# Optimization experiments

Measured on AMD Instinct MI355X. Metric: run time of the kernel, lower is better.

Reference implementation:

```python
import jax, jax.numpy as jnp
import numpy as np

BINS = 256
EPS = 1e-8


def _norm255(x):
    # (x - min) / (max - min) * 255, truncated to int (torch .int())
    mx = jnp.max(x, axis=(2, 3), keepdims=True)
    mn = jnp.min(x, axis=(2, 3), keepdims=True)
    return ((x - mn) / (mx - mn) * 255.0).astype(jnp.int32)


def _hist256(x):
    # x int32 [B,C,H,W] -> per-(b,c) 256-bin histogram [B,C,256] float32
    B, C = x.shape[0], x.shape[1]
    flat = x.reshape(B * C, -1)
    rows = jnp.arange(B * C)[:, None]
    h = jnp.zeros((B * C, BINS), jnp.float32).at[rows, flat].add(1.0)
    return h.reshape(B, C, BINS)


def _entropy(x):
    # faithful to Entropy(): p = hist / (H*W); h = -sum p*log(p+1e-8)
    B, C, H, W = x.shape
    p = _hist256(x) / (H * W)
    h = -jnp.sum(p * jnp.log(p + EPS), axis=2)
    return h[:, :, None, None]  # [B,C,1,1]


def _joint_entropy(x_p, x_ms):
    # Faithful to Joint_entropy's quirky count: for each (i,j) it counts pixels
    # where (x_ms==i AND x_p==j) OR (x_ms!=i AND x_p!=j).
    # count[i,j] = 2*J[i,j] + npix - hist_ms[i] - hist_p[j], J = joint histogram.
    B, C, H, W = x_ms.shape
    npix = H * W
    bins = jnp.arange(BINS)
    M = (x_ms.reshape(B, C, npix)[..., None] == bins).astype(jnp.float32)  # [B,C,P,256]
    P = (x_p.reshape(B, npix)[..., None] == bins).astype(jnp.float32)      # [B,P,256]
    J = jnp.einsum('bcpi,bpj->bcij', M, P)                                  # [B,C,256,256]
    hist_ms = jnp.sum(M, axis=2)  # [B,C,256]
    hist_p = jnp.sum(P, axis=1)   # [B,256]
    count = 2.0 * J + npix - hist_ms[:, :, :, None] - hist_p[:, None, None, :]
    p = count / float(BINS * BINS)  # original divides by 256*256, not npix
    h = -jnp.sum(p * jnp.log(p + EPS), axis=(2, 3))
    return h[:, :, None, None]  # [B,C,1,1]


def _channel(f_p, f_ms):
    B, C, H, W = f_p.shape
    f_p_m = jnp.mean(f_p, axis=1, keepdims=True)  # [B,1,H,W]
    # AdaptiveAvgPool2d((16,16)) with H,W divisible by 16 == block mean
    pooled = f_p.reshape(B, C, 16, H // 16, 16, W // 16).mean(axis=(3, 5))
    f_p_a = jnp.mean(pooled, axis=1, keepdims=True)  # [B,1,16,16]
    f_ms_n = _norm255(f_ms)
    f_p_m_n = _norm255(f_p_m)
    f_p_a_n = _norm255(f_p_a)
    h_ms = _entropy(f_ms_n)                 # [B,C,1,1]
    h_p = _entropy(f_p_m_n)                 # [B,1,1,1]
    h_ms_p = _joint_entropy(f_p_a_n, f_ms_n)  # [B,C,1,1]
    mi = h_p + h_ms - h_ms_p
    mi = jax.nn.softmax(mi, axis=1)  # nn.Softmax() on 4D -> dim=1
    return f_ms + f_ms * mi


def _similarity(f_p, f_ms):
    B, C, H, W = f_p.shape
    f_ms_u = jax.image.resize(f_ms, (B, C, H, W), method='bilinear')
    a = f_ms_u.reshape(B, C, -1)
    b = f_p.reshape(B, C, -1)
    a = a - jnp.mean(a, axis=2, keepdims=True)
    b = b - jnp.mean(b, axis=2, keepdims=True)
    na = jnp.sqrt(jnp.sum(a * a, axis=2))  # [B,C] (ms norms)
    nb = jnp.sqrt(jnp.sum(b * b, axis=2))  # [B,C] (p norms)
    s = jnp.einsum('bcp,bdp->bcd', a, b)   # [B,C,C]
    return s / ((na * nb) / 100.0)[:, :, None]


def _spatial(f_p, f_ms):
    B, C, H, W = f_p.shape
    s_m = _similarity(f_p, f_ms)
    mx = jnp.max(s_m, axis=2)        # [B,C]
    idx = jnp.argmax(s_m, axis=2)    # [B,C] best f_p channel per ms channel
    scores = jax.nn.softmax(mx, axis=1)
    brow = jnp.arange(B)[:, None]
    # group score: sum of softmax scores of ms-channels that picked value v
    g = jnp.zeros((B, C), scores.dtype).at[brow, idx].add(scores)
    cnt = jnp.zeros((B, C), jnp.int32).at[brow, idx].add(1)
    k = jnp.min(jnp.sum(cnt > 0, axis=1))  # min #unique over batch
    min_k = (k + 1) // 2                   # ceil(min_k / 2)
    order = jnp.argsort(-g, axis=1)        # descending group score; absent groups (0) sort last
    sorted_scores = jnp.take_along_axis(g, order, axis=1)  # [B,C]
    pos_mask = jnp.arange(C) < min_k       # keep top min_k positions
    z = jnp.where(pos_mask[None, :], sorted_scores, -jnp.inf)
    w = jax.nn.softmax(z, axis=1)          # softmax over selected scores, 0 elsewhere
    gathered = jnp.take_along_axis(f_p, order[:, :, None, None], axis=1)  # [B,C,H,W]
    mask = jnp.sum(w[:, :, None, None] * jax.nn.sigmoid(gathered), axis=1, keepdims=True)
    return f_p + f_p * mask


def setup_inputs() -> dict:
    key = jax.random.key(0)
    k1, k2 = jax.random.split(key)
    f_p = jax.random.normal(k1, (8, 64, 256, 256), dtype=jnp.float32)
    f_ms = jax.random.normal(k2, (8, 64, 16, 16), dtype=jnp.float32)
    return {"f_p": f_p, "f_ms": f_ms}


def reference(f_p, f_ms):
    rel_ms = _channel(f_p, f_ms)
    rel_p = _spatial(f_p, f_ms)
    return (rel_p, rel_ms)
```

## Files before the change

### kernel.cpp

```cpp
#include <hip/hip_runtime.h>

#define BB 8
#define CC 64
#define HP 256
#define WP 256
#define PP 65536
#define QQ 256

__device__ __forceinline__ unsigned encF(float f) {
    unsigned u = __float_as_uint(f);
    return (u & 0x80000000u) ? ~u : (u | 0x80000000u);
}
__device__ __forceinline__ float decF(unsigned u) {
    unsigned b = (u & 0x80000000u) ? (u ^ 0x80000000u) : ~u;
    return __uint_as_float(b);
}

__device__ __forceinline__ double blockSumD(double v, double* red4) {
    int t = threadIdx.x;
    for (int d = 32; d; d >>= 1) v += __shfl_down(v, d, 64);
    __syncthreads();
    if ((t & 63) == 0) red4[t >> 6] = v;
    __syncthreads();
    double r = red4[0] + red4[1] + red4[2] + red4[3];
    __syncthreads();
    return r;
}

__global__ void k0_init(unsigned* minmax, int* histpm) {
    int t = threadIdx.x + blockIdx.x * blockDim.x;
    if (t < BB) { minmax[2 * t] = 0xFFFFFFFFu; minmax[2 * t + 1] = 0u; }
    if (t < BB * 256) histpm[t] = 0;
}

__global__ __launch_bounds__(256) void k1_fpm(const float* __restrict__ fp,
                                              float* __restrict__ fpm,
                                              unsigned* __restrict__ minmax) {
    int b = blockIdx.y;
    int i4 = blockIdx.x * 256 + threadIdx.x;
    const float4* src = (const float4*)(fp + (size_t)b * CC * PP);
    float sx = 0.f, sy = 0.f, sz = 0.f, sw = 0.f;
#pragma unroll 8
    for (int c = 0; c < CC; ++c) {
        float4 v = src[(size_t)c * (PP / 4) + i4];
        sx += v.x; sy += v.y; sz += v.z; sw += v.w;
    }
    const float inv = 1.0f / 64.0f;
    float4 m; m.x = sx * inv; m.y = sy * inv; m.z = sz * inv; m.w = sw * inv;
    ((float4*)(fpm + (size_t)b * PP))[i4] = m;
    float mn = fminf(fminf(m.x, m.y), fminf(m.z, m.w));
    float mx = fmaxf(fmaxf(m.x, m.y), fmaxf(m.z, m.w));
    for (int d = 32; d; d >>= 1) {
        mn = fminf(mn, __shfl_down(mn, d, 64));
        mx = fmaxf(mx, __shfl_down(mx, d, 64));
    }
    __shared__ unsigned smn, smx;
    if (threadIdx.x == 0) { smn = 0xFFFFFFFFu; smx = 0u; }
    __syncthreads();
    if ((threadIdx.x & 63) == 0) { atomicMin(&smn, encF(mn)); atomicMax(&smx, encF(mx)); }
    __syncthreads();
    if (threadIdx.x == 0) { atomicMin(&minmax[2 * b], smn); atomicMax(&minmax[2 * b + 1], smx); }
}

__global__ __launch_bounds__(256) void k2a_hist(const float* __restrict__ fpm,
                                                const unsigned* __restrict__ minmax,
                                                int* __restrict__ histpm) {
    int b = blockIdx.y;
    __shared__ int h[256];
    h[threadIdx.x] = 0;
    __syncthreads();
    float mn = decF(minmax[2 * b]);
    float mx = decF(minmax[2 * b + 1]);
    float dd = mx - mn;
    int i4 = blockIdx.x * 256 + threadIdx.x;
    float4 v = ((const float4*)(fpm + (size_t)b * PP))[i4];
    int b0 = (int)((v.x - mn) / dd * 255.0f);
    int b1 = (int)((v.y - mn) / dd * 255.0f);
    int b2 = (int)((v.z - mn) / dd * 255.0f);
    int b3 = (int)((v.w - mn) / dd * 255.0f);
    b0 = min(max(b0, 0), 255); b1 = min(max(b1, 0), 255);
    b2 = min(max(b2, 0), 255); b3 = min(max(b3, 0), 255);
    atomicAdd(&h[b0], 1); atomicAdd(&h[b1], 1);
    atomicAdd(&h[b2], 1); atomicAdd(&h[b3], 1);
    __syncthreads();
    atomicAdd(&histpm[b * 256 + threadIdx.x], h[threadIdx.x]);
}

__global__ __launch_bounds__(256) void k2b_entropy(const int* __restrict__ histpm,
                                                   float* __restrict__ hpE) {
    __shared__ double red4[4];
    int b = blockIdx.x;
    int n = histpm[b * 256 + threadIdx.x];
    float p = (float)n * (1.0f / 65536.0f);
    double term = -(double)(p * __logf(p + 1e-8f));
    double h = blockSumD(term, red4);
    if (threadIdx.x == 0) hpE[b] = (float)h;
}

__global__ __launch_bounds__(256) void k3_chan(const float* __restrict__ fp,
                                               float* __restrict__ cellsum,
                                               float* __restrict__ gtent,
                                               float* __restrict__ chsum,
                                               float* __restrict__ chsumsq) {
    int blk = blockIdx.x, b = blk >> 6, c = blk & 63;
    int x = threadIdx.x, s = x >> 4, r = x & 15;
    const float* src = fp + (size_t)(b * CC + c) * PP;
    __shared__ float tentL[256];
    __shared__ double red4[4];
    tentL[x] = 0.0f;
    __syncthreads();
    float wm, w0, wp;
    if (x <= 7)        { wm = 0.f; w0 = 1.f; wp = 0.f; }
    else if (x >= 248) { wm = 0.f; w0 = 1.f; wp = 0.f; }
    else if (r < 8)    { float fx = ((float)r + 8.5f) * 0.0625f; wm = 1.f - fx; w0 = fx;       wp = 0.f; }
    else               { float fx = ((float)r - 7.5f) * 0.0625f; wm = 0.f;      w0 = 1.f - fx; wp = fx;  }
    double sum = 0.0, ssq = 0.0;
    for (int q = 0; q < 16; ++q) {
        float am = 0.f, a0 = 0.f, ap = 0.f, cs = 0.f;
#pragma unroll
        for (int ry = 0; ry < 16; ++ry) {
            float v = src[(q * 16 + ry) * 256 + x];
            sum += (double)v;
            ssq += (double)v * (double)v;
            cs  += v;
            if ((q == 0 && ry < 8) || (q == 15 && ry >= 8)) {
                a0 += v;
            } else if (ry < 8) {
                float fy = ((float)ry + 8.5f) * 0.0625f;
                am += (1.f - fy) * v; a0 += fy * v;
            } else {
                float fy = ((float)ry - 7.5f) * 0.0625f;
                a0 += (1.f - fy) * v; ap += fy * v;
            }
        }
        float vals[10];
        vals[0] = am * wm; vals[1] = am * w0; vals[2] = am * wp;
        vals[3] = a0 * wm; vals[4] = a0 * w0; vals[5] = a0 * wp;
        vals[6] = ap * wm; vals[7] = ap * w0; vals[8] = ap * wp;
        vals[9] = cs;
#pragma unroll
        for (int d = 8; d; d >>= 1) {
#pragma unroll
            for (int k2 = 0; k2 < 10; ++k2) vals[k2] += __shfl_down(vals[k2], d, 16);
        }
        if (r == 0) {
            if (q > 0) {
                if (s > 0)  atomicAdd(&tentL[(q - 1) * 16 + (s - 1)], vals[0]);
                atomicAdd(&tentL[(q - 1) * 16 + s], vals[1]);
                if (s < 15) atomicAdd(&tentL[(q - 1) * 16 + (s + 1)], vals[2]);
            }
            if (s > 0)  atomicAdd(&tentL[q * 16 + (s - 1)], vals[3]);
            atomicAdd(&tentL[q * 16 + s], vals[4]);
            if (s < 15) atomicAdd(&tentL[q * 16 + (s + 1)], vals[5]);
            if (q < 15) {
                if (s > 0)  atomicAdd(&tentL[(q + 1) * 16 + (s - 1)], vals[6]);
                atomicAdd(&tentL[(q + 1) * 16 + s], vals[7]);
                if (s < 15) atomicAdd(&tentL[(q + 1) * 16 + (s + 1)], vals[8]);
            }
            cellsum[(size_t)(b * CC + c) * QQ + q * 16 + s] = vals[9];
        }
    }
    __syncthreads();
    gtent[(size_t)(b * CC + c) * QQ + x] = tentL[x];
    double st = blockSumD(sum, red4);
    double sq = blockSumD(ssq, red4);
    if (x == 0) { chsum[b * CC + c] = (float)st; chsumsq[b * CC + c] = (float)sq; }
}

__global__ __launch_bounds__(256) void k4_ms(const float* __restrict__ fms,
                                             int* __restrict__ msn,
                                             int* __restrict__ histms,
                                             float* __restrict__ hmsE,
                                             float* __restrict__ naArr,
                                             float* __restrict__ mssum) {
    int blk = blockIdx.x, b = blk >> 6, c = blk & 63, t = threadIdx.x;
    __shared__ float m[256];
    __shared__ int hist[256];
    __shared__ double red4[4];
    __shared__ double U[256];
    __shared__ unsigned umn, umx;
    float v = fms[(size_t)(b * CC + c) * QQ + t];
    m[t] = v;
    hist[t] = 0;
    if (t == 0) { umn = 0xFFFFFFFFu; umx = 0u; }
    float mn = v, mx = v;
    for (int d = 32; d; d >>= 1) {
        mn = fminf(mn, __shfl_down(mn, d, 64));
        mx = fmaxf(mx, __shfl_down(mx, d, 64));
    }
    __syncthreads();
    if ((t & 63) == 0) { atomicMin(&umn, encF(mn)); atomicMax(&umx, encF(mx)); }
    __syncthreads();
    mn = decF(umn); mx = decF(umx);
    int bin = (int)((v - mn) / (mx - mn) * 255.0f);
    bin = min(max(bin, 0), 255);
    msn[(size_t)(b * CC + c) * QQ + t] = bin;
    atomicAdd(&hist[bin], 1);
    __syncthreads();
    histms[(size_t)(b * CC + c) * QQ + t] = hist[t];
    float pf = (float)hist[t] * (1.0f / 256.0f);
    double term = -(double)(pf * __logf(pf + 1e-8f));
    double h = blockSumD(term, red4);
    if (t == 0) hmsE[b * CC + c] = (float)h;
    int i = t >> 4, j = t & 15;
    double kdj = (j == 0 || j == 15) ? 13.328125 : 10.65625;
    double mv = (double)m[t];
    double uu = kdj * mv + 2.671875 * ((j > 0 ? (double)m[t - 1] : 0.0) +
                                       (j < 15 ? (double)m[t + 1] : 0.0));
    U[t] = uu;
    __syncthreads();
    double kdi = (i == 0 || i == 15) ? 13.328125 : 10.65625;
    double vv = kdi * U[t] + 2.671875 * ((i > 0 ? U[t - 16] : 0.0) +
                                         (i < 15 ? U[t + 16] : 0.0));
    double sq = blockSumD(mv * vv, red4);
    double msm = blockSumD(mv, red4);
    if (t == 0) {
        mssum[b * CC + c] = (float)msm;
        double meanu = msm * (1.0 / 256.0);
        double na2 = sq - 65536.0 * meanu * meanu;
        naArr[b * CC + c] = (float)sqrt(na2 > 0.0 ? na2 : 0.0);
    }
}

__global__ __launch_bounds__(256) void k5_pa(const float* __restrict__ cellsum,
                                             int* __restrict__ pan,
                                             int* __restrict__ histp) {
    int b = blockIdx.x, t = threadIdx.x;
    __shared__ int hist[256];
    __shared__ unsigned umn, umx;
    hist[t] = 0;
    if (t == 0) { umn = 0xFFFFFFFFu; umx = 0u; }
    double acc = 0.0;
    for (int c = 0; c < CC; ++c) acc += (double)cellsum[(size_t)(b * CC + c) * QQ + t];
    float pa = (float)(acc * (1.0 / 256.0) * (1.0 / 64.0));
    float mn = pa, mx = pa;
    for (int d = 32; d; d >>= 1) {
        mn = fminf(mn, __shfl_down(mn, d, 64));
        mx = fmaxf(mx, __shfl_down(mx, d, 64));
    }
    __syncthreads();
    if ((t & 63) == 0) { atomicMin(&umn, encF(mn)); atomicMax(&umx, encF(mx)); }
    __syncthreads();
    mn = decF(umn); mx = decF(umx);
    int bin = (int)((pa - mn) / (mx - mn) * 255.0f);
    bin = min(max(bin, 0), 255);
    pan[b * QQ + t] = bin;
    atomicAdd(&hist[bin], 1);
    __syncthreads();
    histp[b * 256 + t] = hist[t];
}

__global__ __launch_bounds__(256) void k6_joint(const int* __restrict__ msn,
                                                const int* __restrict__ pan,
                                                const int* __restrict__ histms,
                                                const int* __restrict__ histp,
                                                float* __restrict__ hjoint) {
    int blk = blockIdx.x, b = blk >> 6, c = blk & 63, t = threadIdx.x;
    __shared__ int key[256], hms[256], hp[256];
    __shared__ double red4[4];
    int iv = msn[(size_t)(b * CC + c) * QQ + t];
    int jv = pan[b * QQ + t];
    key[t] = (iv << 8) | jv;
    hms[t] = histms[(size_t)(b * CC + c) * QQ + t];
    hp[t] = histp[b * 256 + t];
    __syncthreads();
    unsigned long long w0_ = 0, w1_ = 0, w2_ = 0, w3_ = 0;
    for (int p = 0; p < 256; ++p) {
        int k2 = key[p];
        if ((k2 >> 8) == t) {
            int j = k2 & 255;
            unsigned long long bit = 1ull << (j & 63);
            int w = j >> 6;
            if (w == 0) w0_ |= bit; else if (w == 1) w1_ |= bit;
            else if (w == 2) w2_ |= bit; else w3_ |= bit;
        }
    }
    double acc = 0.0;
    int basei = 256 - hms[t];
    unsigned long long words[4] = { w0_, w1_, w2_, w3_ };
#pragma unroll
    for (int w = 0; w < 4; ++w) {
        unsigned long long word = words[w];
        for (int jj = 0; jj < 64; ++jj) {
            if (!((word >> jj) & 1ull)) {
                int cnt = basei - hp[w * 64 + jj];
                float pf = (float)cnt * (1.0f / 65536.0f);
                acc -= (double)(pf * __logf(pf + 1e-8f));
            }
        }
    }
    int myk = key[t], n = 0; bool first = true;
    for (int p = 0; p < 256; ++p) {
        int k2 = key[p];
        if (k2 == myk) { n++; if (p < t) first = false; }
    }
    if (first) {
        int cnt = 2 * n + 256 - hms[myk >> 8] - hp[myk & 255];
        float pf = (float)cnt * (1.0f / 65536.0f);
        acc -= (double)(pf * __logf(pf + 1e-8f));
    }
    double h = blockSumD(acc, red4);
    if (t == 0) hjoint[b * CC + c] = (float)h;
}

__global__ __launch_bounds__(256) void k7_relms(const float* __restrict__ fms,
                                                const float* __restrict__ hmsE,
                                                const float* __restrict__ hpE,
                                                const float* __restrict__ hjoint,
                                                float* __restrict__ out2) {
    int b = blockIdx.x, t = threadIdx.x;
    __shared__ double mi[64];
    if (t < 64) mi[t] = (double)hpE[b] + (double)hmsE[b * CC + t] - (double)hjoint[b * CC + t];
    __syncthreads();
    if (t == 0) {
        double mxv = mi[0];
        for (int c2 = 1; c2 < 64; ++c2) if (mi[c2] > mxv) mxv = mi[c2];
        double s = 0.0;
        for (int c2 = 0; c2 < 64; ++c2) { mi[c2] = exp(mi[c2] - mxv); s += mi[c2]; }
        for (int c2 = 0; c2 < 64; ++c2) mi[c2] /= s;
    }
    __syncthreads();
    const float* src = fms + (size_t)b * CC * QQ;
    float* dst = out2 + (size_t)b * CC * QQ;
    for (int e = t; e < CC * QQ; e += 256) {
        float v = src[e];
        float miv = (float)mi[e >> 8];
        dst[e] = v + v * miv;
    }
}

__global__ __launch_bounds__(256) void k8_smax(const float* __restrict__ fms,
                                               const float* __restrict__ gtent,
                                               const float* __restrict__ mssum,
                                               const float* __restrict__ chsum,
                                               const float* __restrict__ chsumsq,
                                               const float* __restrict__ naArr,
                                               float* __restrict__ mxArr,
                                               int* __restrict__ idxArr) {
    int blk = blockIdx.x, b = blk >> 6, c = blk & 63, t = threadIdx.x;
    __shared__ float msrow[256];
    __shared__ double part[256];
    __shared__ double sval[64];
    msrow[t] = fms[(size_t)(b * CC + c) * QQ + t];
    __syncthreads();
    int d = t >> 2, pr = t & 3;
    const float* g = gtent + (size_t)(b * CC + d) * QQ + pr * 64;
    const float* mr = msrow + pr * 64;
    double acc = 0.0;
    for (int q2 = 0; q2 < 64; ++q2) acc += (double)mr[q2] * (double)g[q2];
    part[t] = acc;
    __syncthreads();
    if (t < 64) {
        double meanu = (double)mssum[b * CC + c] * (1.0 / 256.0);
        double meanp = (double)chsum[b * CC + t] * (1.0 / 65536.0);
        sval[t] = part[t * 4] + part[t * 4 + 1] + part[t * 4 + 2] + part[t * 4 + 3]
                  - 65536.0 * meanu * meanp;
    }
    __syncthreads();
    if (t == 0) {
        double best = sval[0]; int bi2 = 0;
        for (int dd = 1; dd < 64; ++dd) { if (sval[dd] > best) { best = sval[dd]; bi2 = dd; } }
        double nac = (double)naArr[b * CC + c];
        double sc_ = (double)chsum[b * CC + c];
        double sq_ = (double)chsumsq[b * CC + c];
        double nb2 = sq_ - sc_ * sc_ * (1.0 / 65536.0);
        double nbc = sqrt(nb2 > 0.0 ? nb2 : 0.0);
        mxArr[b * CC + c] = (float)(best * 100.0 / (nac * nbc));
        idxArr[b * CC + c] = bi2;
    }
}

__global__ __launch_bounds__(512) void k9_small(const float* __restrict__ mxArr,
                                                const int* __restrict__ idxArr,
                                                float* __restrict__ wsel,
                                                int* __restrict__ chanA,
                                                int* __restrict__ minkA) {
    __shared__ double sc[8][64];
    __shared__ double gs[8][64];
    __shared__ int idxS[8][64];
    __shared__ int ordv[8][64];
    __shared__ int uarr[8];
    __shared__ int mkS;
    int t = threadIdx.x;
    int b = t >> 6, c = t & 63;
    double v = (double)mxArr[b * 64 + c];
    double mx = v;
    for (int d = 32; d; d >>= 1) mx = fmax(mx, __shfl_down(mx, d, 64));
    mx = __shfl(mx, 0, 64);
    double e = exp(v - mx);
    double s = e;
    for (int d = 32; d; d >>= 1) s += __shfl_down(s, d, 64);
    s = __shfl(s, 0, 64);
    sc[b][c] = e / s;
    idxS[b][c] = idxArr[b * 64 + c];
    __syncthreads();
    double g = 0.0; int cnt = 0;
    for (int c2 = 0; c2 < 64; ++c2) {
        if (idxS[b][c2] == c) { g += sc[b][c2]; cnt++; }
    }
    gs[b][c] = g;
    unsigned long long ball = __ballot(cnt > 0);
    if (c == 0) uarr[b] = __popcll(ball);
    __syncthreads();
    if (t == 0) {
        int k = uarr[0];
        for (int b2 = 1; b2 < 8; ++b2) k = min(k, uarr[b2]);
        mkS = (k + 1) >> 1;
        minkA[0] = mkS;
    }
    __syncthreads();
    int rk = 0;
    double myg = gs[b][c];
    for (int c3 = 0; c3 < 64; ++c3) {
        double a = gs[b][c3];
        if (a > myg || (a == myg && c3 < c)) rk++;
    }
    ordv[b][rk] = c;
    __syncthreads();
    int mk = mkS;
    double z0 = gs[b][ordv[b][0]];
    double ee = (c < mk) ? exp(gs[b][ordv[b][c]] - z0) : 0.0;
    double se = ee;
    for (int d = 32; d; d >>= 1) se += __shfl_down(se, d, 64);
    se = __shfl(se, 0, 64);
    if (c < mk) {
        wsel[b * 64 + c] = (float)(ee / se);
        chanA[b * 64 + c] = ordv[b][c];
    }
}

__global__ __launch_bounds__(256) void k10_relp(const float* __restrict__ fp,
                                                const float* __restrict__ wsel,
                                                const int* __restrict__ chanA,
                                                const int* __restrict__ minkA,
                                                float* __restrict__ outp) {
    int b = blockIdx.y;
    int i4 = blockIdx.x * 256 + threadIdx.x;
    int mk = minkA[0];
    const float4* src = (const float4*)(fp + (size_t)b * CC * PP);
    float mx0 = 0.f, mx1 = 0.f, mx2 = 0.f, mx3 = 0.f;
    for (int i = 0; i < mk; ++i) {
        int ch = chanA[b * 64 + i];
        float wv = wsel[b * 64 + i];
        float4 v = src[(size_t)ch * (PP / 4) + i4];
        mx0 += wv * (1.0f / (1.0f + __expf(-v.x)));
        mx1 += wv * (1.0f / (1.0f + __expf(-v.y)));
        mx2 += wv * (1.0f / (1.0f + __expf(-v.z)));
        mx3 += wv * (1.0f / (1.0f + __expf(-v.w)));
    }
    float4* dst = (float4*)(outp + (size_t)b * CC * PP);
    for (int c2 = 0; c2 < CC; ++c2) {
        float4 v = src[(size_t)c2 * (PP / 4) + i4];
        float4 o;
        o.x = v.x + v.x * mx0;
        o.y = v.y + v.y * mx1;
        o.z = v.z + v.z * mx2;
        o.w = v.w + v.w * mx3;
        dst[(size_t)c2 * (PP / 4) + i4] = o;
    }
}

extern "C" void kernel_launch(void* const* d_in, const int* in_sizes, int n_in,
                              void* d_out, int out_size, void* d_ws, size_t ws_size,
                              hipStream_t stream) {
    const float* fp = (const float*)d_in[0];
    const float* fms = (const float*)d_in[1];
    float* out = (float*)d_out;

    char* p = (char*)d_ws;
    auto alloc = [&](size_t bytes) { void* r = (void*)p; p += (bytes + 255) & ~(size_t)255; return r; };

    float* fpm      = (float*)alloc((size_t)BB * PP * 4);
    float* cellsum  = (float*)alloc((size_t)BB * CC * QQ * 4);
    float* gtent    = (float*)alloc((size_t)BB * CC * QQ * 4);
    float* chsum    = (float*)alloc((size_t)BB * CC * 4);
    float* chsumsq  = (float*)alloc((size_t)BB * CC * 4);
    unsigned* minmax= (unsigned*)alloc((size_t)BB * 2 * 4);
    int* histpm     = (int*)alloc((size_t)BB * 256 * 4);
    int* msn        = (int*)alloc((size_t)BB * CC * QQ * 4);
    int* histms     = (int*)alloc((size_t)BB * CC * 256 * 4);
    int* histp      = (int*)alloc((size_t)BB * 256 * 4);
    int* pan        = (int*)alloc((size_t)BB * QQ * 4);
    float* hmsE     = (float*)alloc((size_t)BB * CC * 4);
    float* hpE      = (float*)alloc((size_t)BB * 4);
    float* hjoint   = (float*)alloc((size_t)BB * CC * 4);
    float* naArr    = (float*)alloc((size_t)BB * CC * 4);
    float* mssum    = (float*)alloc((size_t)BB * CC * 4);
    float* mxArr    = (float*)alloc((size_t)BB * CC * 4);
    int* idxArr     = (int*)alloc((size_t)BB * CC * 4);
    float* wsel     = (float*)alloc((size_t)BB * CC * 4);
    int* chanA      = (int*)alloc((size_t)BB * CC * 4);
    int* minkA      = (int*)alloc(256);

    float* out_relp  = out;
    float* out_relms = out + (size_t)BB * CC * PP;

    k0_init<<<8, 256, 0, stream>>>(minmax, histpm);
    k1_fpm<<<dim3(64, 8), 256, 0, stream>>>(fp, fpm, minmax);
    k2a_hist<<<dim3(64, 8), 256, 0, stream>>>(fpm, minmax, histpm);
    k2b_entropy<<<8, 256, 0, stream>>>(histpm, hpE);
    k3_chan<<<512, 256, 0, stream>>>(fp, cellsum, gtent, chsum, chsumsq);
    k4_ms<<<512, 256, 0, stream>>>(fms, msn, histms, hmsE, naArr, mssum);
    k5_pa<<<8, 256, 0, stream>>>(cellsum, pan, histp);
    k6_joint<<<512, 256, 0, stream>>>(msn, pan, histms, histp, hjoint);
    k7_relms<<<8, 256, 0, stream>>>(fms, hmsE, hpE, hjoint, out_relms);
    k8_smax<<<512, 256, 0, stream>>>(fms, gtent, mssum, chsum, chsumsq, naArr, mxArr, idxArr);
    k9_small<<<1, 512, 0, stream>>>(mxArr, idxArr, wsel, chanA, minkA);
    k10_relp<<<dim3(64, 8), 256, 0, stream>>>(fp, wsel, chanA, minkA, out_relp);
}
```

Baseline: 414.3 us.

## Replace global atomics with per-block partials, vectorize k3 loads, drop init and entropy kernels

Global atomic min/max and histogram accumulation are replaced by per-block partial arrays that later kernels reduce, which removes the init kernel and folds the fpm entropy into k7. The channel-statistics kernel switches to float4 loads, with each wave handling four row groups. In k10 the selected channel and weight lists are staged in shared memory, and the copy loop is unrolled. The aim is fewer kernel launches and better memory throughput in the bandwidth-bound passes, at the cost of more partial data reread by the consumer kernels.

```diff
diff --git a/kernel.cpp b/kernel.cpp
--- a/kernel.cpp
+++ b/kernel.cpp
@@ -7,15 +7,6 @@
 #define PP 65536
 #define QQ 256
 
-__device__ __forceinline__ unsigned encF(float f) {
-    unsigned u = __float_as_uint(f);
-    return (u & 0x80000000u) ? ~u : (u | 0x80000000u);
-}
-__device__ __forceinline__ float decF(unsigned u) {
-    unsigned b = (u & 0x80000000u) ? (u ^ 0x80000000u) : ~u;
-    return __uint_as_float(b);
-}
-
 __device__ __forceinline__ double blockSumD(double v, double* red4) {
     int t = threadIdx.x;
     for (int d = 32; d; d >>= 1) v += __shfl_down(v, d, 64);
@@ -27,15 +18,9 @@
     return r;
 }
 
-__global__ void k0_init(unsigned* minmax, int* histpm) {
-    int t = threadIdx.x + blockIdx.x * blockDim.x;
-    if (t < BB) { minmax[2 * t] = 0xFFFFFFFFu; minmax[2 * t + 1] = 0u; }
-    if (t < BB * 256) histpm[t] = 0;
-}
-
 __global__ __launch_bounds__(256) void k1_fpm(const float* __restrict__ fp,
                                               float* __restrict__ fpm,
-                                              unsigned* __restrict__ minmax) {
+                                              float* __restrict__ pminmax) {
     int b = blockIdx.y;
     int i4 = blockIdx.x * 256 + threadIdx.x;
     const float4* src = (const float4*)(fp + (size_t)b * CC * PP);
@@ -54,23 +39,30 @@
         mn = fminf(mn, __shfl_down(mn, d, 64));
         mx = fmaxf(mx, __shfl_down(mx, d, 64));
     }
-    __shared__ unsigned smn, smx;
-    if (threadIdx.x == 0) { smn = 0xFFFFFFFFu; smx = 0u; }
-    __syncthreads();
-    if ((threadIdx.x & 63) == 0) { atomicMin(&smn, encF(mn)); atomicMax(&smx, encF(mx)); }
-    __syncthreads();
-    if (threadIdx.x == 0) { atomicMin(&minmax[2 * b], smn); atomicMax(&minmax[2 * b + 1], smx); }
+    __shared__ float smn[4], smx[4];
+    if ((threadIdx.x & 63) == 0) { smn[threadIdx.x >> 6] = mn; smx[threadIdx.x >> 6] = mx; }
+    __syncthreads();
+    if (threadIdx.x == 0) {
+        float a = fminf(fminf(smn[0], smn[1]), fminf(smn[2], smn[3]));
+        float z = fmaxf(fmaxf(smx[0], smx[1]), fmaxf(smx[2], smx[3]));
+        pminmax[2 * (b * 64 + blockIdx.x)] = a;
+        pminmax[2 * (b * 64 + blockIdx.x) + 1] = z;
+    }
 }
 
 __global__ __launch_bounds__(256) void k2a_hist(const float* __restrict__ fpm,
-                                                const unsigned* __restrict__ minmax,
-                                                int* __restrict__ histpm) {
+                                                const float* __restrict__ pminmax,
+                                                int* __restrict__ histpart) {
     int b = blockIdx.y;
     __shared__ int h[256];
     h[threadIdx.x] = 0;
     __syncthreads();
-    float mn = decF(minmax[2 * b]);
-    float mx = decF(minmax[2 * b + 1]);
+    float mn = 1e30f, mx = -1e30f;
+#pragma unroll 8
+    for (int k = 0; k < 64; ++k) {
+        mn = fminf(mn, pminmax[2 * (b * 64 + k)]);
+        mx = fmaxf(mx, pminmax[2 * (b * 64 + k) + 1]);
+    }
     float dd = mx - mn;
     int i4 = blockIdx.x * 256 + threadIdx.x;
     float4 v = ((const float4*)(fpm + (size_t)b * PP))[i4];
@@ -83,18 +75,7 @@
     atomicAdd(&h[b0], 1); atomicAdd(&h[b1], 1);
     atomicAdd(&h[b2], 1); atomicAdd(&h[b3], 1);
     __syncthreads();
-    atomicAdd(&histpm[b * 256 + threadIdx.x], h[threadIdx.x]);
-}
-
-__global__ __launch_bounds__(256) void k2b_entropy(const int* __restrict__ histpm,
-                                                   float* __restrict__ hpE) {
-    __shared__ double red4[4];
-    int b = blockIdx.x;
-    int n = histpm[b * 256 + threadIdx.x];
-    float p = (float)n * (1.0f / 65536.0f);
-    double term = -(double)(p * __logf(p + 1e-8f));
-    double h = blockSumD(term, red4);
-    if (threadIdx.x == 0) hpE[b] = (float)h;
+    histpart[(size_t)(b * 64 + blockIdx.x) * 256 + threadIdx.x] = h[threadIdx.x];
 }
 
 __global__ __launch_bounds__(256) void k3_chan(const float* __restrict__ fp,
@@ -103,47 +84,65 @@
                                                float* __restrict__ chsum,
                                                float* __restrict__ chsumsq) {
     int blk = blockIdx.x, b = blk >> 6, c = blk & 63;
-    int x = threadIdx.x, s = x >> 4, r = x & 15;
-    const float* src = fp + (size_t)(b * CC + c) * PP;
+    int t = threadIdx.x;
+    int wave = t >> 6;
+    int j = t & 63;
+    int s = j >> 2;
+    const float4* src = (const float4*)(fp + (size_t)(b * CC + c) * PP);
     __shared__ float tentL[256];
     __shared__ double red4[4];
-    tentL[x] = 0.0f;
-    __syncthreads();
-    float wm, w0, wp;
-    if (x <= 7)        { wm = 0.f; w0 = 1.f; wp = 0.f; }
-    else if (x >= 248) { wm = 0.f; w0 = 1.f; wp = 0.f; }
-    else if (r < 8)    { float fx = ((float)r + 8.5f) * 0.0625f; wm = 1.f - fx; w0 = fx;       wp = 0.f; }
-    else               { float fx = ((float)r - 7.5f) * 0.0625f; wm = 0.f;      w0 = 1.f - fx; wp = fx;  }
+    tentL[t] = 0.0f;
+    __syncthreads();
+    float wmv[4], w0v[4], wpv[4];
+#pragma unroll
+    for (int k = 0; k < 4; ++k) {
+        int col = 4 * j + k, r = col & 15;
+        if (col <= 7 || col >= 248)      { wmv[k] = 0.f; w0v[k] = 1.f; wpv[k] = 0.f; }
+        else if (r < 8) { float fx = ((float)r + 8.5f) * 0.0625f; wmv[k] = 1.f - fx; w0v[k] = fx;       wpv[k] = 0.f; }
+        else            { float fx = ((float)r - 7.5f) * 0.0625f; wmv[k] = 0.f;      w0v[k] = 1.f - fx; wpv[k] = fx;  }
+    }
     double sum = 0.0, ssq = 0.0;
-    for (int q = 0; q < 16; ++q) {
-        float am = 0.f, a0 = 0.f, ap = 0.f, cs = 0.f;
+    for (int qq = 0; qq < 4; ++qq) {
+        int q = wave * 4 + qq;
+        float amx = 0.f, amy = 0.f, amz = 0.f, amw = 0.f;
+        float a0x = 0.f, a0y = 0.f, a0z = 0.f, a0w = 0.f;
+        float apx = 0.f, apy = 0.f, apz = 0.f, apw = 0.f;
+        float csx = 0.f, csy = 0.f, csz = 0.f, csw = 0.f;
 #pragma unroll
         for (int ry = 0; ry < 16; ++ry) {
-            float v = src[(q * 16 + ry) * 256 + x];
-            sum += (double)v;
-            ssq += (double)v * (double)v;
-            cs  += v;
+            float4 v = src[(q * 16 + ry) * 64 + j];
+            sum += (double)v.x + (double)v.y + (double)v.z + (double)v.w;
+            ssq += (double)v.x * v.x + (double)v.y * v.y + (double)v.z * v.z + (double)v.w * v.w;
+            csx += v.x; csy += v.y; csz += v.z; csw += v.w;
             if ((q == 0 && ry < 8) || (q == 15 && ry >= 8)) {
-                a0 += v;
+                a0x += v.x; a0y += v.y; a0z += v.z; a0w += v.w;
             } else if (ry < 8) {
-                float fy = ((float)ry + 8.5f) * 0.0625f;
-                am += (1.f - fy) * v; a0 += fy * v;
+                float fy = ((float)ry + 8.5f) * 0.0625f; float gy = 1.f - fy;
+                amx += gy * v.x; amy += gy * v.y; amz += gy * v.z; amw += gy * v.w;
+                a0x += fy * v.x; a0y += fy * v.y; a0z += fy * v.z; a0w += fy * v.w;
             } else {
-                float fy = ((float)ry - 7.5f) * 0.0625f;
-                a0 += (1.f - fy) * v; ap += fy * v;
+                float fy = ((float)ry - 7.5f) * 0.0625f; float gy = 1.f - fy;
+                a0x += gy * v.x; a0y += gy * v.y; a0z += gy * v.z; a0w += gy * v.w;
+                apx += fy * v.x; apy += fy * v.y; apz += fy * v.z; apw += fy * v.w;
             }
         }
         float vals[10];
-        vals[0] = am * wm; vals[1] = am * w0; vals[2] = am * wp;
-        vals[3] = a0 * wm; vals[4] = a0 * w0; vals[5] = a0 * wp;
-        vals[6] = ap * wm; vals[7] = ap * w0; vals[8] = ap * wp;
-        vals[9] = cs;
+        vals[0] = amx * wmv[0] + amy * wmv[1] + amz * wmv[2] + amw * wmv[3];
+        vals[1] = amx * w0v[0] + amy * w0v[1] + amz * w0v[2] + amw * w0v[3];
+        vals[2] = amx * wpv[0] + amy * wpv[1] + amz * wpv[2] + amw * wpv[3];
+        vals[3] = a0x * wmv[0] + a0y * wmv[1] + a0z * wmv[2] + a0w * wmv[3];
+        vals[4] = a0x * w0v[0] + a0y * w0v[1] + a0z * w0v[2] + a0w * w0v[3];
+        vals[5] = a0x * wpv[0] + a0y * wpv[1] + a0z * wpv[2] + a0w * wpv[3];
+        vals[6] = apx * wmv[0] + apy * wmv[1] + apz * wmv[2] + apw * wmv[3];
+        vals[7] = apx * w0v[0] + apy * w0v[1] + apz * w0v[2] + apw * w0v[3];
+        vals[8] = apx * wpv[0] + apy * wpv[1] + apz * wpv[2] + apw * wpv[3];
+        vals[9] = csx + csy + csz + csw;
 #pragma unroll
-        for (int d = 8; d; d >>= 1) {
-#pragma unroll
-            for (int k2 = 0; k2 < 10; ++k2) vals[k2] += __shfl_down(vals[k2], d, 16);
+        for (int k2 = 0; k2 < 10; ++k2) {
+            vals[k2] += __shfl_down(vals[k2], 2, 4);
+            vals[k2] += __shfl_down(vals[k2], 1, 4);
         }
-        if (r == 0) {
+        if ((j & 3) == 0) {
             if (q > 0) {
                 if (s > 0)  atomicAdd(&tentL[(q - 1) * 16 + (s - 1)], vals[0]);
                 atomicAdd(&tentL[(q - 1) * 16 + s], vals[1]);
@@ -161,10 +160,10 @@
         }
     }
     __syncthreads();
-    gtent[(size_t)(b * CC + c) * QQ + x] = tentL[x];
+    gtent[(size_t)(b * CC + c) * QQ + t] = tentL[t];
     double st = blockSumD(sum, red4);
     double sq = blockSumD(ssq, red4);
-    if (x == 0) { chsum[b * CC + c] = (float)st; chsumsq[b * CC + c] = (float)sq; }
+    if (t == 0) { chsum[b * CC + c] = (float)st; chsumsq[b * CC + c] = (float)sq; }
 }
 
 __global__ __launch_bounds__(256) void k4_ms(const float* __restrict__ fms,
@@ -178,20 +177,19 @@
     __shared__ int hist[256];
     __shared__ double red4[4];
     __shared__ double U[256];
-    __shared__ unsigned umn, umx;
+    __shared__ float smn[4], smx[4];
     float v = fms[(size_t)(b * CC + c) * QQ + t];
     m[t] = v;
     hist[t] = 0;
-    if (t == 0) { umn = 0xFFFFFFFFu; umx = 0u; }
     float mn = v, mx = v;
     for (int d = 32; d; d >>= 1) {
         mn = fminf(mn, __shfl_down(mn, d, 64));
         mx = fmaxf(mx, __shfl_down(mx, d, 64));
     }
-    __syncthreads();
-    if ((t & 63) == 0) { atomicMin(&umn, encF(mn)); atomicMax(&umx, encF(mx)); }
-    __syncthreads();
-    mn = decF(umn); mx = decF(umx);
+    if ((t & 63) == 0) { smn[t >> 6] = mn; smx[t >> 6] = mx; }
+    __syncthreads();
+    mn = fminf(fminf(smn[0], smn[1]), fminf(smn[2], smn[3]));
+    mx = fmaxf(fmaxf(smx[0], smx[1]), fmaxf(smx[2], smx[3]));
     int bin = (int)((v - mn) / (mx - mn) * 255.0f);
     bin = min(max(bin, 0), 255);
     msn[(size_t)(b * CC + c) * QQ + t] = bin;
@@ -227,9 +225,8 @@
                                              int* __restrict__ histp) {
     int b = blockIdx.x, t = threadIdx.x;
     __shared__ int hist[256];
-    __shared__ unsigned umn, umx;
+    __shared__ float smn[4], smx[4];
     hist[t] = 0;
-    if (t == 0) { umn = 0xFFFFFFFFu; umx = 0u; }
     double acc = 0.0;
     for (int c = 0; c < CC; ++c) acc += (double)cellsum[(size_t)(b * CC + c) * QQ + t];
     float pa = (float)(acc * (1.0 / 256.0) * (1.0 / 64.0));
@@ -238,10 +235,10 @@
         mn = fminf(mn, __shfl_down(mn, d, 64));
         mx = fmaxf(mx, __shfl_down(mx, d, 64));
     }
-    __syncthreads();
-    if ((t & 63) == 0) { atomicMin(&umn, encF(mn)); atomicMax(&umx, encF(mx)); }
-    __syncthreads();
-    mn = decF(umn); mx = decF(umx);
+    if ((t & 63) == 0) { smn[t >> 6] = mn; smx[t >> 6] = mx; }
+    __syncthreads();
+    mn = fminf(fminf(smn[0], smn[1]), fminf(smn[2], smn[3]));
+    mx = fmaxf(fmaxf(smx[0], smx[1]), fmaxf(smx[2], smx[3]));
     int bin = (int)((pa - mn) / (mx - mn) * 255.0f);
     bin = min(max(bin, 0), 255);
     pan[b * QQ + t] = bin;
@@ -305,12 +302,22 @@
 
 __global__ __launch_bounds__(256) void k7_relms(const float* __restrict__ fms,
                                                 const float* __restrict__ hmsE,
-                                                const float* __restrict__ hpE,
+                                                const int* __restrict__ histpart,
                                                 const float* __restrict__ hjoint,
                                                 float* __restrict__ out2) {
     int b = blockIdx.x, t = threadIdx.x;
+    __shared__ double red4[4];
     __shared__ double mi[64];
-    if (t < 64) mi[t] = (double)hpE[b] + (double)hmsE[b * CC + t] - (double)hjoint[b * CC + t];
+    __shared__ double hpS;
+    int n = 0;
+#pragma unroll 8
+    for (int k = 0; k < 64; ++k) n += histpart[(size_t)(b * 64 + k) * 256 + t];
+    float pp = (float)n * (1.0f / 65536.0f);
+    double term = -(double)(pp * __logf(pp + 1e-8f));
+    double hpE = blockSumD(term, red4);
+    if (t == 0) hpS = hpE;
+    __syncthreads();
+    if (t < 64) mi[t] = hpS + (double)hmsE[b * CC + t] - (double)hjoint[b * CC + t];
     __syncthreads();
     if (t == 0) {
         double mxv = mi[0];
@@ -436,12 +443,18 @@
                                                 float* __restrict__ outp) {
     int b = blockIdx.y;
     int i4 = blockIdx.x * 256 + threadIdx.x;
-    int mk = minkA[0];
+    __shared__ float wS[64];
+    __shared__ int cS[64];
+    __shared__ int mkL;
+    if (threadIdx.x < 64) { wS[threadIdx.x] = wsel[b * 64 + threadIdx.x]; cS[threadIdx.x] = chanA[b * 64 + threadIdx.x]; }
+    if (threadIdx.x == 0) mkL = minkA[0];
+    __syncthreads();
+    int mk = mkL;
     const float4* src = (const float4*)(fp + (size_t)b * CC * PP);
     float mx0 = 0.f, mx1 = 0.f, mx2 = 0.f, mx3 = 0.f;
     for (int i = 0; i < mk; ++i) {
-        int ch = chanA[b * 64 + i];
-        float wv = wsel[b * 64 + i];
+        int ch = cS[i];
+        float wv = wS[i];
         float4 v = src[(size_t)ch * (PP / 4) + i4];
         mx0 += wv * (1.0f / (1.0f + __expf(-v.x)));
         mx1 += wv * (1.0f / (1.0f + __expf(-v.y)));
@@ -449,6 +462,7 @@
         mx3 += wv * (1.0f / (1.0f + __expf(-v.w)));
     }
     float4* dst = (float4*)(outp + (size_t)b * CC * PP);
+#pragma unroll 4
     for (int c2 = 0; c2 < CC; ++c2) {
         float4 v = src[(size_t)c2 * (PP / 4) + i4];
         float4 o;
@@ -475,14 +489,13 @@
     float* gtent    = (float*)alloc((size_t)BB * CC * QQ * 4);
     float* chsum    = (float*)alloc((size_t)BB * CC * 4);
     float* chsumsq  = (float*)alloc((size_t)BB * CC * 4);
-    unsigned* minmax= (unsigned*)alloc((size_t)BB * 2 * 4);
-    int* histpm     = (int*)alloc((size_t)BB * 256 * 4);
+    float* pminmax  = (float*)alloc((size_t)BB * 64 * 2 * 4);
+    int* histpart   = (int*)alloc((size_t)BB * 64 * 256 * 4);
     int* msn        = (int*)alloc((size_t)BB * CC * QQ * 4);
     int* histms     = (int*)alloc((size_t)BB * CC * 256 * 4);
     int* histp      = (int*)alloc((size_t)BB * 256 * 4);
     int* pan        = (int*)alloc((size_t)BB * QQ * 4);
     float* hmsE     = (float*)alloc((size_t)BB * CC * 4);
-    float* hpE      = (float*)alloc((size_t)BB * 4);
     float* hjoint   = (float*)alloc((size_t)BB * CC * 4);
     float* naArr    = (float*)alloc((size_t)BB * CC * 4);
     float* mssum    = (float*)alloc((size_t)BB * CC * 4);
@@ -495,15 +508,13 @@
     float* out_relp  = out;
     float* out_relms = out + (size_t)BB * CC * PP;
 
-    k0_init<<<8, 256, 0, stream>>>(minmax, histpm);
-    k1_fpm<<<dim3(64, 8), 256, 0, stream>>>(fp, fpm, minmax);
-    k2a_hist<<<dim3(64, 8), 256, 0, stream>>>(fpm, minmax, histpm);
-    k2b_entropy<<<8, 256, 0, stream>>>(histpm, hpE);
+    k1_fpm<<<dim3(64, 8), 256, 0, stream>>>(fp, fpm, pminmax);
+    k2a_hist<<<dim3(64, 8), 256, 0, stream>>>(fpm, pminmax, histpart);
     k3_chan<<<512, 256, 0, stream>>>(fp, cellsum, gtent, chsum, chsumsq);
     k4_ms<<<512, 256, 0, stream>>>(fms, msn, histms, hmsE, naArr, mssum);
     k5_pa<<<8, 256, 0, stream>>>(cellsum, pan, histp);
     k6_joint<<<512, 256, 0, stream>>>(msn, pan, histms, histp, hjoint);
-    k7_relms<<<8, 256, 0, stream>>>(fms, hmsE, hpE, hjoint, out_relms);
+    k7_relms<<<8, 256, 0, stream>>>(fms, hmsE, histpart, hjoint, out_relms);
     k8_smax<<<512, 256, 0, stream>>>(fms, gtent, mssum, chsum, chsumsq, naArr, mxArr, idxArr);
     k9_small<<<1, 512, 0, stream>>>(mxArr, idxArr, wsel, chanA, minkA);
     k10_relp<<<dim3(64, 8), 256, 0, stream>>>(fp, wsel, chanA, minkA, out_relp);
```

Measured after the change: 417.7 us. No clear change (+0.8%).
